# Performance work log

Hardware: AMD Instinct MI355X
Metric: run time of the kernel (lower is better)

The kernel has to match this reference:

```python
import jax, jax.numpy as jnp
import numpy as np

HID = 3584      # hidden_size
NQ = 16         # num query heads
NKV = 8         # num kv heads
D = 256         # head_dim
SCALE = 256.0 ** -0.5   # query_pre_attn_scalar ** -0.5
CAP = 50.0      # attn_logits_soft_cap
WINDOW = 2048   # interleaved sliding window (even layer)
THETA = 10000.0
B, S = 1, 4096


def _rope(x, positions):
    """Neox-style RoPE. x: [B,S,N,D], positions: [B,S] int."""
    half = D // 2
    inv_freq = 1.0 / (THETA ** (jnp.arange(half, dtype=jnp.float32) / half))
    freqs = positions.astype(jnp.float32)[:, :, None] * inv_freq  # [B,S,half]
    cos = jnp.cos(freqs)[:, :, None, :]  # [B,S,1,half]
    sin = jnp.sin(freqs)[:, :, None, :]
    x1, x2 = x[..., :half], x[..., half:]
    return jnp.concatenate([x1 * cos - x2 * sin, x2 * cos + x1 * sin], axis=-1)


def setup_inputs() -> dict:
    key = jax.random.key(0)
    k1, k2, k3 = jax.random.split(key, 3)
    positions = jnp.broadcast_to(jnp.arange(S, dtype=jnp.int64)[None, :], (B, S))
    hidden_states = jax.random.normal(k1, (B, S, HID), dtype=jnp.float32)
    # scale weights ~ 1/sqrt(fan_in) so activations are O(1)
    w_qkv = jax.random.normal(k2, ((NQ + 2 * NKV) * D, HID), dtype=jnp.float32) * (HID ** -0.5)
    w_o = jax.random.normal(k3, (HID, NQ * D), dtype=jnp.float32) * ((NQ * D) ** -0.5)
    return {"positions": positions, "hidden_states": hidden_states, "w_qkv": w_qkv, "w_o": w_o}


def reference(positions, hidden_states, w_qkv, w_o):
    q_size, kv_size = NQ * D, NKV * D
    qkv = jnp.einsum('bsh,oh->bso', hidden_states, w_qkv)
    q = qkv[..., :q_size].reshape(B, S, NQ, D)
    k = qkv[..., q_size:q_size + kv_size].reshape(B, S, NKV, D)
    v = qkv[..., q_size + kv_size:].reshape(B, S, NKV, D)
    q = _rope(q, positions)
    k = _rope(k, positions)
    # GQA: repeat kv heads to match query heads
    g = NQ // NKV
    k = jnp.repeat(k, g, axis=2)  # [B,S,NQ,D]
    v = jnp.repeat(v, g, axis=2)
    scores = jnp.einsum('bqhd,bkhd->bhqk', q, k) * SCALE
    # Gemma2 logit soft-capping
    scores = CAP * jnp.tanh(scores / CAP)
    i = jnp.arange(S)[:, None]
    j = jnp.arange(S)[None, :]
    mask = (j <= i) & (i - j < WINDOW)  # causal + sliding window
    scores = jnp.where(mask, scores, -1e30)
    probs = jax.nn.softmax(scores, axis=-1)
    attn = jnp.einsum('bhqk,bkhd->bqhd', probs, v).reshape(B, S, NQ * D)
    return jnp.einsum('bso,ho->bsh', attn, w_o)
```

## Files before the change

### kernel.cpp

```cpp
#include <hip/hip_runtime.h>
#include <hip/hip_bf16.h>

typedef __bf16 bf16_t;
typedef __bf16 bf16x4 __attribute__((ext_vector_type(4)));
typedef __bf16 bf16x8 __attribute__((ext_vector_type(8)));
typedef float f32x4 __attribute__((ext_vector_type(4)));

#define HIDDEN 3584
#define NQH 16
#define NKVH 8
#define DH 256
#define SEQ 4096
#define QKV_COLS 8192
#define Q_SIZE 4096
#define KV_SIZE 2048
#define WINDOW 2048
#define SCALE_F 0.0625f
#define CAP_F 50.0f

__device__ __forceinline__ void gload16(const bf16_t* g, bf16_t* l) {
  __builtin_amdgcn_global_load_lds((__attribute__((address_space(1))) void*)g,
                                   (__attribute__((address_space(3))) void*)l, 16, 0, 0);
}

__global__ __launch_bounds__(256) void cvt_all(const float* __restrict__ hid,
                                               const float* __restrict__ wqkv,
                                               const float* __restrict__ wo,
                                               bf16_t* __restrict__ hb,
                                               bf16_t* __restrict__ qb,
                                               bf16_t* __restrict__ wb) {
  long i = (long)blockIdx.x * 256 + threadIdx.x;
  const float* src;
  bf16_t* dst;
  long off;
  if (i < 1835008)       { src = hid;  dst = hb; off = i; }
  else if (i < 5505024)  { src = wqkv; dst = qb; off = i - 1835008; }
  else                   { src = wo;   dst = wb; off = i - 5505024; }
  const float4* s4 = (const float4*)src;
  float4 a = s4[off * 2];
  float4 b = s4[off * 2 + 1];
  bf16x8 o;
  o[0] = (bf16_t)a.x; o[1] = (bf16_t)a.y; o[2] = (bf16_t)a.z; o[3] = (bf16_t)a.w;
  o[4] = (bf16_t)b.x; o[5] = (bf16_t)b.y; o[6] = (bf16_t)b.z; o[7] = (bf16_t)b.w;
  *(bf16x8*)(dst + off * 8) = o;
}

#define TILE(T, WSTR, STAGE)                                                                \
  {                                                                                         \
    char* buf = lds + ((T) & 3) * 32768;                                                    \
    bf16x8 af[8], b0, b1, b2, b3;                                                           \
    _Pragma("unroll")                                                                       \
    for (int i = 0; i < 8; ++i) af[i] = *(const bf16x8*)(buf + aoff + i * 1024);            \
    b0 = *(const bf16x8*)(buf + boff);                                                      \
    b1 = *(const bf16x8*)(buf + boff + 1024);                                               \
    if (STAGE) {                                                                            \
      char* d = lds + (((T) + 3) & 3) * 32768;                                              \
      gload16(sA0 + ((T) + 3) * 32, (bf16_t*)(d + sdst0));                                  \
      gload16(sA1 + ((T) + 3) * 32, (bf16_t*)(d + 8192 + sdst0));                           \
    }                                                                                       \
    __builtin_amdgcn_s_setprio(1);                                                          \
    _Pragma("unroll")                                                                       \
    for (int i = 0; i < 8; ++i) {                                                           \
      acc[i][0] = __builtin_amdgcn_mfma_f32_16x16x32_bf16(af[i], b0, acc[i][0], 0, 0, 0);   \
      acc[i][1] = __builtin_amdgcn_mfma_f32_16x16x32_bf16(af[i], b1, acc[i][1], 0, 0, 0);   \
    }                                                                                       \
    __builtin_amdgcn_s_setprio(0);                                                          \
    b2 = *(const bf16x8*)(buf + boff + 2048);                                               \
    b3 = *(const bf16x8*)(buf + boff + 3072);                                               \
    if (STAGE) {                                                                            \
      char* d = lds + (((T) + 3) & 3) * 32768;                                              \
      gload16(sB0 + ((T) + 3) * 32, (bf16_t*)(d + 16384 + sdst0));                          \
      gload16(sB1 + ((T) + 3) * 32, (bf16_t*)(d + 24576 + sdst0));                          \
    }                                                                                       \
    __builtin_amdgcn_s_setprio(1);                                                          \
    _Pragma("unroll")                                                                       \
    for (int i = 0; i < 8; ++i) {                                                           \
      acc[i][2] = __builtin_amdgcn_mfma_f32_16x16x32_bf16(af[i], b2, acc[i][2], 0, 0, 0);   \
      acc[i][3] = __builtin_amdgcn_mfma_f32_16x16x32_bf16(af[i], b3, acc[i][3], 0, 0, 0);   \
    }                                                                                       \
    __builtin_amdgcn_s_setprio(0);                                                          \
    asm volatile("s_waitcnt vmcnt(" WSTR ")" ::: "memory");                                 \
    __builtin_amdgcn_s_barrier();                                                           \
  }

template <int K, int MODE>
__global__ __launch_bounds__(512, 2) void gemm_bt(const bf16_t* __restrict__ A,
                                                  const bf16_t* __restrict__ B,
                                                  void* __restrict__ Cout,
                                                  bf16_t* __restrict__ vtout, int N) {
  constexpr int NT = K / 32;
  __shared__ char lds[4 * 32768];
  int tid = threadIdx.x;
  int lane = tid & 63, w = tid >> 6;
  int wm = w >> 2, wn = w & 3;
  int r16 = lane & 15, g = lane >> 4;
  int bid = blockIdx.x;
  long bm = (long)((bid & 7) * 2 + ((bid >> 3) & 1)) * 256;
  long bn = (long)(bid >> 4) * 256;
  int ro = r16 >> 1;
  int asl = ((g + ((r16 & 1) << 2)) ^ ro) << 4;
  int aoff = wm * 8192 + ro * 128 + asl;
  int boff = 16384 + wn * 4096 + ro * 128 + asl;
  int slr = lane >> 3;
  int lc = (lane & 7) ^ slr;
  int kc8 = (lc & 3) * 8;
  long mr0 = (long)(w * 8 + slr) * 2 + (lc >> 2);
  long mr1 = mr0 + 128;
  const bf16_t* sA0 = A + (bm + mr0) * K + kc8;
  const bf16_t* sA1 = A + (bm + mr1) * K + kc8;
  const bf16_t* sB0 = B + (bn + mr0) * K + kc8;
  const bf16_t* sB1 = B + (bn + mr1) * K + kc8;
  int sdst0 = w * 1024;
  f32x4 acc[8][4] = {};
#pragma unroll
  for (int u = 0; u < 3; ++u) {
    char* d = lds + u * 32768;
    gload16(sA0 + u * 32, (bf16_t*)(d + sdst0));
    gload16(sA1 + u * 32, (bf16_t*)(d + 8192 + sdst0));
    gload16(sB0 + u * 32, (bf16_t*)(d + 16384 + sdst0));
    gload16(sB1 + u * 32, (bf16_t*)(d + 24576 + sdst0));
  }
  asm volatile("s_waitcnt vmcnt(8)" ::: "memory");
  __builtin_amdgcn_s_barrier();
  int t = 0;
  for (; t < NT - 3; ++t) TILE(t, "8", true);
  TILE(t, "4", false); ++t;
  TILE(t, "0", false); ++t;
  TILE(t, "0", false);
  if (MODE == 1 && bn >= (Q_SIZE + KV_SIZE)) {
#pragma unroll
    for (int i = 0; i < 8; ++i) {
      long row = bm + wm * 128 + i * 16 + g * 4;
#pragma unroll
      for (int j = 0; j < 4; ++j) {
        long colv = bn - (Q_SIZE + KV_SIZE) + wn * 64 + j * 16 + r16;
        bf16x4 o;
#pragma unroll
        for (int r = 0; r < 4; ++r) o[r] = (bf16_t)acc[i][j][r];
        *(bf16x4*)&vtout[colv * SEQ + row] = o;
      }
    }
  } else {
#pragma unroll
    for (int i = 0; i < 8; ++i)
#pragma unroll
      for (int j = 0; j < 4; ++j)
#pragma unroll
        for (int r = 0; r < 4; ++r) {
          long row = bm + wm * 128 + i * 16 + g * 4 + r;
          long col = bn + wn * 64 + j * 16 + r16;
          if (MODE == 1) ((bf16_t*)Cout)[row * N + col] = (bf16_t)acc[i][j][r];
          else           ((float*)Cout)[row * N + col]  = acc[i][j][r];
        }
  }
}

__global__ __launch_bounds__(256) void rope_k_kernel(bf16_t* __restrict__ qkv) {
  long idx = (long)blockIdx.x * 256 + threadIdx.x;
  int i8 = (int)(idx & 15) * 8;
  long rem = idx >> 4;
  int head = (int)(rem & 7);
  int s = (int)(rem >> 3);
  long p1 = (long)s * QKV_COLS + Q_SIZE + head * DH + i8;
  bf16x8 x1 = *(const bf16x8*)&qkv[p1];
  bf16x8 x2 = *(const bf16x8*)&qkv[p1 + 128];
  bf16x8 o1, o2;
#pragma unroll
  for (int j = 0; j < 8; ++j) {
    float inv_freq = exp2f((float)(i8 + j) * -0.10381025296522976f);
    float fr = (float)s * inv_freq;
    float sn, cs;
    sincosf(fr, &sn, &cs);
    float a = (float)x1[j], b = (float)x2[j];
    o1[j] = (bf16_t)(a * cs - b * sn);
    o2[j] = (bf16_t)(b * cs + a * sn);
  }
  *(bf16x8*)&qkv[p1] = o1;
  *(bf16x8*)&qkv[p1 + 128] = o2;
}

__global__ __launch_bounds__(512, 2) void attn_kernel(const bf16_t* __restrict__ qkv,
                                                      const bf16_t* __restrict__ vt,
                                                      bf16_t* __restrict__ attn_out) {
  __shared__ bf16_t Kb[2][64 * 256];
  __shared__ bf16_t Vb[2][256 * 64];
  __shared__ bf16_t Pl[8 * 1024];
  int tid = threadIdx.x;
  int lane = tid & 63, w = tid >> 6;
  int r16 = lane & 15, g = lane >> 4;
  int bid = blockIdx.x;
  int swz = (bid & 7) * 64 + (bid >> 3);
  int h = swz >> 5;
  int qb0 = swz & 31;
  int qb = (h & 1) ? (31 - qb0) : qb0;
  int kvh = h >> 1;
  int qw = qb * 128 + w * 16;
  bf16x8 qf[8];
  long qoff = (long)(qw + r16) * QKV_COLS + h * DH + g * 8;
#pragma unroll
  for (int kk = 0; kk < 8; ++kk) qf[kk] = *(const bf16x8*)&qkv[qoff + kk * 32];
#pragma unroll
  for (int kk = 0; kk < 4; ++kk)
#pragma unroll
    for (int j = 0; j < 8; ++j) {
      int d = kk * 32 + g * 8 + j;
      float inv_freq = exp2f((float)d * -0.10381025296522976f);
      float fr = (float)(qw + r16) * inv_freq;
      float sn, cs;
      sincosf(fr, &sn, &cs);
      float a = (float)qf[kk][j], b2 = (float)qf[kk + 4][j];
      qf[kk][j] = (bf16_t)(a * cs - b2 * sn);
      qf[kk + 4][j] = (bf16_t)(b2 * cs + a * sn);
    }
  f32x4 acc[16] = {};
  float lsum[4] = {};
  const bf16_t* kg = qkv + Q_SIZE + (long)kvh * DH;
  const bf16_t* vg = vt + (long)kvh * DH * SEQ;
  bf16_t* pw = Pl + w * 1024;
  int lo = qb * 128 - (WINDOW - 1);
  int t0 = lo > 0 ? (lo >> 6) : 0;
  int t1 = qb * 2 + 2;
  int qlo = qw, qhi = qw + 15;

#define ATTN_STAGE(TT)                                                                   \
  {                                                                                      \
    int b_ = (TT) & 1;                                                                   \
    int kb_ = (TT) * 64;                                                                 \
    _Pragma("unroll")                                                                    \
    for (int c = 0; c < 4; ++c) {                                                        \
      int rowk = w * 8 + c * 2 + (lane >> 5);                                            \
      gload16(kg + (long)(kb_ + rowk) * QKV_COLS + (((lane & 31) ^ (rowk & 7)) * 8),     \
              &Kb[b_][w * 2048 + c * 512]);                                              \
      int rowv = w * 32 + c * 8 + (lane >> 3);                                           \
      gload16(vg + (long)rowv * SEQ + kb_ + (((lane & 7) ^ (rowv & 7)) * 8),             \
              &Vb[b_][w * 2048 + c * 512]);                                              \
    }                                                                                    \
  }

  ATTN_STAGE(t0);
  __syncthreads();
  for (int tt = t0; tt < t1; ++tt) {
    if (tt + 1 < t1) ATTN_STAGE(tt + 1);
    int b = tt & 1;
    int kb = tt * 64;
    bool active = !(kb > qhi || kb + 63 < qlo - (WINDOW - 1));
    if (active) {
      bool full = (kb + 63 <= qlo) && (qhi - kb <= WINDOW - 1);
      f32x4 sc[4] = {};
      __builtin_amdgcn_s_setprio(1);
#pragma unroll
      for (int kk = 0; kk < 8; ++kk) {
        int sl = ((kk * 4 + g) ^ (r16 & 7)) * 8;
#pragma unroll
        for (int c = 0; c < 4; ++c) {
          bf16x8 kf = *(const bf16x8*)&Kb[b][(c * 16 + r16) * 256 + sl];
          sc[c] = __builtin_amdgcn_mfma_f32_16x16x32_bf16(qf[kk], kf, sc[c], 0, 0, 0);
        }
      }
      __builtin_amdgcn_s_setprio(0);
#pragma unroll
      for (int c = 0; c < 4; ++c)
#pragma unroll
        for (int r = 0; r < 4; ++r) {
          float s = sc[c][r];
          float e = __expf(s * (2.0f * SCALE_F / CAP_F));
          float rr = __builtin_amdgcn_rcpf(e + 1.0f);
          float p = __expf(fmaf(-100.0f, rr, 38.0f));
          if (!full) {
            int q = qw + g * 4 + r;
            int k = kb + c * 16 + r16;
            p = ((k <= q) && (q - k < WINDOW)) ? p : 0.0f;
          }
          lsum[r] += p;
          int prow = g * 4 + r;
          int pbyte = prow * 128 + ((c * 32 + r16 * 2) ^ ((prow & 7) << 4));
          *(bf16_t*)((char*)pw + pbyte) = (bf16_t)p;
        }
      bf16x8 pa[2];
#pragma unroll
      for (int pk = 0; pk < 2; ++pk) {
        int pb = r16 * 128 + ((pk * 64 + g * 16) ^ ((r16 & 7) << 4));
        pa[pk] = *(const bf16x8*)((const char*)pw + pb);
      }
      __builtin_amdgcn_s_setprio(1);
#pragma unroll
      for (int dt = 0; dt < 16; ++dt) {
        int vrow = (dt * 16 + r16) * 64;
        bf16x8 vf0 = *(const bf16x8*)&Vb[b][vrow + ((g ^ (r16 & 7)) * 8)];
        acc[dt] = __builtin_amdgcn_mfma_f32_16x16x32_bf16(pa[0], vf0, acc[dt], 0, 0, 0);
        bf16x8 vf1 = *(const bf16x8*)&Vb[b][vrow + (((4 + g) ^ (r16 & 7)) * 8)];
        acc[dt] = __builtin_amdgcn_mfma_f32_16x16x32_bf16(pa[1], vf1, acc[dt], 0, 0, 0);
      }
      __builtin_amdgcn_s_setprio(0);
    }
    __syncthreads();
  }
  float inv[4];
#pragma unroll
  for (int r = 0; r < 4; ++r) {
    float s = lsum[r];
    s += __shfl_xor(s, 1);
    s += __shfl_xor(s, 2);
    s += __shfl_xor(s, 4);
    s += __shfl_xor(s, 8);
    inv[r] = 1.0f / s;
  }
#pragma unroll
  for (int dt = 0; dt < 16; ++dt)
#pragma unroll
    for (int r = 0; r < 4; ++r) {
      long row = qw + g * 4 + r;
      attn_out[row * Q_SIZE + h * DH + dt * 16 + r16] = (bf16_t)(acc[dt][r] * inv[r]);
    }
}

extern "C" void kernel_launch(void* const* d_in, const int* in_sizes, int n_in,
                              void* d_out, int out_size, void* d_ws, size_t ws_size,
                              hipStream_t stream) {
  const float* hid_f  = (const float*)d_in[1];
  const float* wqkv_f = (const float*)d_in[2];
  const float* wo_f   = (const float*)d_in[3];
  float* out = (float*)d_out;
  char* ws = (char*)d_ws;
  bf16_t* qkv    = (bf16_t*)(ws);
  bf16_t* wo_b   = (bf16_t*)(ws + 67108864);
  bf16_t* hid_b  = (bf16_t*)(ws + 96468992);
  bf16_t* wqkv_b = (bf16_t*)(ws + 125829120);
  bf16_t* attn_b = (bf16_t*)(ws + 96468992);
  bf16_t* vt     = (bf16_t*)d_out;

  cvt_all<<<28672, 256, 0, stream>>>(hid_f, wqkv_f, wo_f, hid_b, wqkv_b, wo_b);
  gemm_bt<HIDDEN, 1><<<512, 512, 0, stream>>>(hid_b, wqkv_b, qkv, vt, QKV_COLS);
  rope_k_kernel<<<2048, 256, 0, stream>>>(qkv);
  attn_kernel<<<512, 512, 0, stream>>>(qkv, vt, attn_b);
  gemm_bt<Q_SIZE, 0><<<224, 512, 0, stream>>>(attn_b, wo_b, out, nullptr, HIDDEN);
}
```

Before: 569.6 us.

## Switch attention to 32x32x16 MFMA with wave pairs splitting keys and head dim

Restructures the attention kernel so each pair of waves handles 32 query rows with 32x32x16 MFMAs instead of one wave per 16 rows with 16x16x32. For QK^T each wave of the pair computes scores for half of the 64 keys; for PV each wave computes half of the head dim, and the two waves share P through LDS with a barrier in between. Row sums are merged across the pair through a small LDS buffer at the end. The goal is fewer K/V LDS reads per MFMA and higher MFMA throughput, at the cost of an extra block barrier per tile and more registers for the 16-wide Q fragments.

After: 797.9 us. 1.4x slower.

```diff
diff --git a/kernel.cpp b/kernel.cpp
--- a/kernel.cpp
+++ b/kernel.cpp
@@ -5,6 +5,7 @@
 typedef __bf16 bf16x4 __attribute__((ext_vector_type(4)));
 typedef __bf16 bf16x8 __attribute__((ext_vector_type(8)));
 typedef float f32x4 __attribute__((ext_vector_type(4)));
+typedef float f32x16 __attribute__((ext_vector_type(16)));
 
 #define HIDDEN 3584
 #define NQH 16
@@ -184,43 +185,45 @@
                                                       bf16_t* __restrict__ attn_out) {
   __shared__ bf16_t Kb[2][64 * 256];
   __shared__ bf16_t Vb[2][256 * 64];
-  __shared__ bf16_t Pl[8 * 1024];
+  __shared__ bf16_t Pl[4][32 * 72];
+  __shared__ float  Ls[4][2][32];
   int tid = threadIdx.x;
   int lane = tid & 63, w = tid >> 6;
-  int r16 = lane & 15, g = lane >> 4;
+  int l31 = lane & 31, hi = lane >> 5;
+  int qg = w >> 1, dh = w & 1;
   int bid = blockIdx.x;
   int swz = (bid & 7) * 64 + (bid >> 3);
   int h = swz >> 5;
   int qb0 = swz & 31;
   int qb = (h & 1) ? (31 - qb0) : qb0;
   int kvh = h >> 1;
-  int qw = qb * 128 + w * 16;
-  bf16x8 qf[8];
-  long qoff = (long)(qw + r16) * QKV_COLS + h * DH + g * 8;
-#pragma unroll
-  for (int kk = 0; kk < 8; ++kk) qf[kk] = *(const bf16x8*)&qkv[qoff + kk * 32];
-#pragma unroll
-  for (int kk = 0; kk < 4; ++kk)
+  int qw = qb * 128 + qg * 32;
+  bf16x8 qf[16];
+  long qoff = (long)(qw + l31) * QKV_COLS + h * DH + hi * 8;
+#pragma unroll
+  for (int ks = 0; ks < 16; ++ks) qf[ks] = *(const bf16x8*)&qkv[qoff + ks * 16];
+#pragma unroll
+  for (int ks = 0; ks < 8; ++ks)
 #pragma unroll
     for (int j = 0; j < 8; ++j) {
-      int d = kk * 32 + g * 8 + j;
+      int d = ks * 16 + hi * 8 + j;
       float inv_freq = exp2f((float)d * -0.10381025296522976f);
-      float fr = (float)(qw + r16) * inv_freq;
+      float fr = (float)(qw + l31) * inv_freq;
       float sn, cs;
       sincosf(fr, &sn, &cs);
-      float a = (float)qf[kk][j], b2 = (float)qf[kk + 4][j];
-      qf[kk][j] = (bf16_t)(a * cs - b2 * sn);
-      qf[kk + 4][j] = (bf16_t)(b2 * cs + a * sn);
-    }
-  f32x4 acc[16] = {};
-  float lsum[4] = {};
+      float a = (float)qf[ks][j], b2 = (float)qf[ks + 8][j];
+      qf[ks][j] = (bf16_t)(a * cs - b2 * sn);
+      qf[ks + 8][j] = (bf16_t)(b2 * cs + a * sn);
+    }
+  f32x16 acc[4] = {};
+  float lsum16[16] = {};
   const bf16_t* kg = qkv + Q_SIZE + (long)kvh * DH;
   const bf16_t* vg = vt + (long)kvh * DH * SEQ;
-  bf16_t* pw = Pl + w * 1024;
+  bf16_t* pw = &Pl[qg][0];
   int lo = qb * 128 - (WINDOW - 1);
   int t0 = lo > 0 ? (lo >> 6) : 0;
   int t1 = qb * 2 + 2;
-  int qlo = qw, qhi = qw + 15;
+  int qlo = qw, qhi = qw + 31;
 
 #define ATTN_STAGE(TT)                                                                   \
   {                                                                                      \
@@ -246,72 +249,81 @@
     bool active = !(kb > qhi || kb + 63 < qlo - (WINDOW - 1));
     if (active) {
       bool full = (kb + 63 <= qlo) && (qhi - kb <= WINDOW - 1);
-      f32x4 sc[4] = {};
+      f32x16 sc = {0.f, 0.f, 0.f, 0.f, 0.f, 0.f, 0.f, 0.f,
+                   0.f, 0.f, 0.f, 0.f, 0.f, 0.f, 0.f, 0.f};
+      int key = dh * 32 + l31;
       __builtin_amdgcn_s_setprio(1);
 #pragma unroll
-      for (int kk = 0; kk < 8; ++kk) {
-        int sl = ((kk * 4 + g) ^ (r16 & 7)) * 8;
-#pragma unroll
-        for (int c = 0; c < 4; ++c) {
-          bf16x8 kf = *(const bf16x8*)&Kb[b][(c * 16 + r16) * 256 + sl];
-          sc[c] = __builtin_amdgcn_mfma_f32_16x16x32_bf16(qf[kk], kf, sc[c], 0, 0, 0);
+      for (int ks = 0; ks < 16; ++ks) {
+        bf16x8 kf = *(const bf16x8*)&Kb[b][key * 256 + (((2 * ks + hi) ^ (lane & 7)) * 8)];
+        sc = __builtin_amdgcn_mfma_f32_32x32x16_bf16(qf[ks], kf, sc, 0, 0, 0);
+      }
+      __builtin_amdgcn_s_setprio(0);
+#pragma unroll
+      for (int reg = 0; reg < 16; ++reg) {
+        int ql = (reg & 3) + 8 * (reg >> 2) + 4 * hi;
+        float s = sc[reg];
+        float e = __expf(s * (2.0f * SCALE_F / CAP_F));
+        float rr = __builtin_amdgcn_rcpf(e + 1.0f);
+        float p = __expf(fmaf(-100.0f, rr, 38.0f));
+        if (!full) {
+          int q = qw + ql;
+          int k = kb + key;
+          p = ((k <= q) && (q - k < WINDOW)) ? p : 0.0f;
+        }
+        lsum16[reg] += p;
+        pw[ql * 72 + key] = (bf16_t)p;
+      }
+    }
+    asm volatile("s_waitcnt lgkmcnt(0)" ::: "memory");
+    __builtin_amdgcn_s_barrier();
+    __builtin_amdgcn_sched_barrier(0);
+    if (active) {
+      bf16x8 pa[4];
+#pragma unroll
+      for (int ks = 0; ks < 4; ++ks)
+        pa[ks] = *(const bf16x8*)&pw[l31 * 72 + ks * 16 + hi * 8];
+      __builtin_amdgcn_s_setprio(1);
+#pragma unroll
+      for (int dt = 0; dt < 4; ++dt) {
+        int d = dh * 128 + dt * 32 + l31;
+#pragma unroll
+        for (int ks = 0; ks < 4; ++ks) {
+          bf16x8 vf = *(const bf16x8*)&Vb[b][d * 64 + (((2 * ks + hi) ^ (lane & 7)) * 8)];
+          acc[dt] = __builtin_amdgcn_mfma_f32_32x32x16_bf16(pa[ks], vf, acc[dt], 0, 0, 0);
         }
       }
       __builtin_amdgcn_s_setprio(0);
-#pragma unroll
-      for (int c = 0; c < 4; ++c)
-#pragma unroll
-        for (int r = 0; r < 4; ++r) {
-          float s = sc[c][r];
-          float e = __expf(s * (2.0f * SCALE_F / CAP_F));
-          float rr = __builtin_amdgcn_rcpf(e + 1.0f);
-          float p = __expf(fmaf(-100.0f, rr, 38.0f));
-          if (!full) {
-            int q = qw + g * 4 + r;
-            int k = kb + c * 16 + r16;
-            p = ((k <= q) && (q - k < WINDOW)) ? p : 0.0f;
-          }
-          lsum[r] += p;
-          int prow = g * 4 + r;
-          int pbyte = prow * 128 + ((c * 32 + r16 * 2) ^ ((prow & 7) << 4));
-          *(bf16_t*)((char*)pw + pbyte) = (bf16_t)p;
-        }
-      bf16x8 pa[2];
-#pragma unroll
-      for (int pk = 0; pk < 2; ++pk) {
-        int pb = r16 * 128 + ((pk * 64 + g * 16) ^ ((r16 & 7) << 4));
-        pa[pk] = *(const bf16x8*)((const char*)pw + pb);
-      }
-      __builtin_amdgcn_s_setprio(1);
-#pragma unroll
-      for (int dt = 0; dt < 16; ++dt) {
-        int vrow = (dt * 16 + r16) * 64;
-        bf16x8 vf0 = *(const bf16x8*)&Vb[b][vrow + ((g ^ (r16 & 7)) * 8)];
-        acc[dt] = __builtin_amdgcn_mfma_f32_16x16x32_bf16(pa[0], vf0, acc[dt], 0, 0, 0);
-        bf16x8 vf1 = *(const bf16x8*)&Vb[b][vrow + (((4 + g) ^ (r16 & 7)) * 8)];
-        acc[dt] = __builtin_amdgcn_mfma_f32_16x16x32_bf16(pa[1], vf1, acc[dt], 0, 0, 0);
-      }
-      __builtin_amdgcn_s_setprio(0);
     }
     __syncthreads();
   }
-  float inv[4];
-#pragma unroll
-  for (int r = 0; r < 4; ++r) {
-    float s = lsum[r];
+#pragma unroll
+  for (int reg = 0; reg < 16; ++reg) {
+    float s = lsum16[reg];
     s += __shfl_xor(s, 1);
     s += __shfl_xor(s, 2);
     s += __shfl_xor(s, 4);
     s += __shfl_xor(s, 8);
-    inv[r] = 1.0f / s;
-  }
-#pragma unroll
-  for (int dt = 0; dt < 16; ++dt)
-#pragma unroll
-    for (int r = 0; r < 4; ++r) {
-      long row = qw + g * 4 + r;
-      attn_out[row * Q_SIZE + h * DH + dt * 16 + r16] = (bf16_t)(acc[dt][r] * inv[r]);
-    }
+    s += __shfl_xor(s, 16);
+    lsum16[reg] = s;
+  }
+  if (l31 == 0) {
+#pragma unroll
+    for (int reg = 0; reg < 16; ++reg)
+      Ls[qg][dh][(reg & 3) + 8 * (reg >> 2) + 4 * hi] = lsum16[reg];
+  }
+  __syncthreads();
+#pragma unroll
+  for (int reg = 0; reg < 16; ++reg) {
+    int ql = (reg & 3) + 8 * (reg >> 2) + 4 * hi;
+    float inv = 1.0f / (lsum16[reg] + Ls[qg][1 - dh][ql]);
+    long row = qw + ql;
+#pragma unroll
+    for (int dt = 0; dt < 4; ++dt) {
+      attn_out[row * Q_SIZE + h * DH + dh * 128 + dt * 32 + l31] =
+          (bf16_t)(acc[dt][reg] * inv);
+    }
+  }
 }
 
 extern "C" void kernel_launch(void* const* d_in, const int* in_sizes, int n_in,
```
